# Kernel optimization log

Hardware: AMD Instinct MI355X
Metric: run time of the kernel (lower is better)

Reference implementation:

```python
import jax, jax.numpy as jnp
import numpy as np
from jax import lax

D_MODEL = 1024
STATE_DIM = 512
BATCH = 4
SEQ_LEN = 8192


def _cayley_eigenvalues(a_params, n):
    # a_full = [0, a_1..a_half, -a_half-1..., antisymmetric tail]
    half = n // 2
    a_full = jnp.zeros((n,), dtype=a_params.dtype)
    a_full = a_full.at[1:half + 1].set(a_params)
    a_full = a_full.at[half + 1:].set(-a_params[::-1][: n - half - 1])
    a_hat = jnp.fft.fft(a_full)            # complex64
    omega = jnp.imag(a_hat)                # (n,), float32
    ones = jnp.ones_like(omega)
    num = lax.complex(ones, -omega)
    den = lax.complex(ones, omega)
    return num / den                        # (n,), |lambda|=1


def setup_inputs() -> dict:
    key = jax.random.key(0)
    k1, k2, k3, k4 = jax.random.split(key, 4)
    u = jax.random.normal(k1, (BATCH, SEQ_LEN, D_MODEL), dtype=jnp.float32)
    a_params = jax.random.normal(k2, (STATE_DIM // 2,), dtype=jnp.float32) * 0.1
    # torch Linear weights: B.weight (state_dim, d_model), C.weight (d_model, state_dim)
    B_w = jax.random.normal(k3, (STATE_DIM, D_MODEL), dtype=jnp.float32) / np.sqrt(D_MODEL)
    C_w = jax.random.normal(k4, (D_MODEL, STATE_DIM), dtype=jnp.float32) / np.sqrt(STATE_DIM)
    D = jnp.ones((D_MODEL,), dtype=jnp.float32)
    return {"u": u, "a_params": a_params, "B_w": B_w, "C_w": C_w, "D": D}


def reference(u, a_params, B_w, C_w, D):
    batch, seq_len, d = u.shape
    n = B_w.shape[0]
    # 1) input projection: (b, t, n)
    Bu = jnp.einsum("btd,nd->btn", u, B_w)
    # 2) per-channel geometric kernel k_j[t] = lambda_j^t
    eig = _cayley_eigenvalues(a_params, n)                 # (n,) complex64
    t = jnp.arange(seq_len, dtype=jnp.float32)
    kernel = jnp.exp(t[:, None] * jnp.log(eig)[None, :])   # (T, n) complex64
    # 3) causal convolution via FFT with next-pow2(2T) padding
    fft_len = 1
    while fft_len < 2 * seq_len:
        fft_len *= 2
    pad = fft_len - seq_len
    kernel_padded = jnp.pad(kernel, ((0, pad), (0, 0)))
    K_hat = jnp.fft.fft(kernel_padded, axis=0)             # (F, n)
    Bu_padded = jnp.pad(Bu, ((0, 0), (0, pad), (0, 0))).astype(jnp.complex64)
    Bu_hat = jnp.fft.fft(Bu_padded, axis=1)                # (b, F, n)
    h = jnp.fft.ifft(K_hat[None] * Bu_hat, axis=1).real[:, :seq_len, :]
    # 4) output projection + skip
    y = jnp.einsum("btn,dn->btd", h, C_w) + D * u
    return y
```

## Files before the change

kernel.cpp:

```cpp
#include <hip/hip_runtime.h>
#include <cstdint>
#include <cstddef>

#define D_MODEL   1024
#define STATE_DIM 512
#define BATCH     4
#define SEQ_LEN   8192
#define M_TOTAL   (BATCH * SEQ_LEN)

typedef unsigned short ushort_t;
typedef __attribute__((ext_vector_type(8))) __bf16 bf16x8;
typedef __attribute__((ext_vector_type(4))) float  f32x4;


__device__ inline ushort_t f2bf(float f) {
  union { float f; uint32_t u; } v; v.f = f;
  uint32_t u = v.u;
  uint32_t r = (u + 0x7FFFu + ((u >> 16) & 1u)) >> 16;
  return (ushort_t)r;
}

__device__ inline float bf2f(ushort_t b) {
  union { uint32_t u; float f; } v; v.u = ((uint32_t)b) << 16;
  return v.f;
}

__device__ inline void llds16(const void* g, void* l) {
  __builtin_amdgcn_global_load_lds(
      (__attribute__((address_space(1))) void*)(void*)g,
      (__attribute__((address_space(3))) void*)l,
      16, 0, 0);
}


__global__ void convert_f32_bf16(const float* __restrict__ in,
                                 ushort_t* __restrict__ out, int n4) {
  int i = blockIdx.x * blockDim.x + threadIdx.x;
  if (i >= n4) return;
  const float4 v = ((const float4*)in)[i];
  ushort4 o;
  o.x = f2bf(v.x); o.y = f2bf(v.y); o.z = f2bf(v.z); o.w = f2bf(v.w);
  ((ushort4*)out)[i] = o;
}


#define NCHUNK 128
#define CLEN   64
#define SOFF   (BATCH * NCHUNK * STATE_DIM)

__global__ __launch_bounds__(64)
void eigen_kernel(const float* __restrict__ a_params, float* __restrict__ lam) {
  const int k = blockIdx.x;
  const int l = threadIdx.x;
  const float c = 6.283185307179586f / 512.0f;
  float om = 0.f;
#pragma unroll
  for (int s = 0; s < 8; ++s) {
    const int n = s * 64 + l;
    float v = 0.f;
    if (n >= 1 && n <= STATE_DIM / 2)      v = a_params[n - 1];
    else if (n > STATE_DIM / 2)            v = -a_params[STATE_DIM - n];
    const int p = (k * n) & 511;
    om -= v * sinf(c * (float)p);
  }
#pragma unroll
  for (int off = 32; off; off >>= 1) om += __shfl_down(om, off);
  if (l == 0) {
    const float d  = 1.f / (1.f + om * om);
    const float lr = (1.f - om * om) * d;
    const float li = -2.f * om * d;
    double th = atan2((double)li, (double)lr) * (double)CLEN;
    lam[k]        = lr;
    lam[512 + k]  = li;
    lam[1024 + k] = (float)cos(th);
    lam[1536 + k] = (float)sin(th);
  }
}


template <int KDIM, int NDIM, bool OUT_BF16, bool FUSE_SKIP>
__global__ __launch_bounds__(256, 4)
void gemm_bt(const ushort_t* __restrict__ A,
             const ushort_t* __restrict__ Bw,
             void* __restrict__ outv,
             const ushort_t* __restrict__ skip_b,
             const float* __restrict__ Dvec) {
  __shared__ __align__(16) ushort_t smA[2 * 128 * 32];
  __shared__ __align__(16) ushort_t smB[2 * 128 * 32];
  const int tid    = threadIdx.x;
  const int wave   = tid >> 6, lane = tid & 63;
  const int lane16 = lane & 15, quad = lane >> 4;
  const int wm = (wave & 1) * 64, wn = (wave >> 1) * 64;
  const int row0 = blockIdx.x * 128;
  const int col0 = blockIdx.y * 128;

  f32x4 acc[4][4];
#pragma unroll
  for (int i = 0; i < 4; ++i)
#pragma unroll
    for (int j = 0; j < 4; ++j) {
      f32x4 z = {0.f, 0.f, 0.f, 0.f};
      acc[i][j] = z;
    }

  const int s_r0 = tid >> 2;
  const int s_c0 = (tid & 3) ^ ((s_r0 >> 1) & 3);
  const int s_r1 = (256 + tid) >> 2;
  const int s_c1 = (tid & 3) ^ ((s_r1 >> 1) & 3);
  const int o0 = (wave * 64) * 16;
  const int o1 = (256 + wave * 64) * 16;

  const ushort_t* gA0 = A  + (size_t)(row0 + s_r0) * KDIM + s_c0 * 8;
  const ushort_t* gB0 = Bw + (size_t)(col0 + s_r0) * KDIM + s_c0 * 8;
  const ushort_t* gA1 = A  + (size_t)(row0 + s_r1) * KDIM + s_c1 * 8;
  const ushort_t* gB1 = Bw + (size_t)(col0 + s_r1) * KDIM + s_c1 * 8;

#define STAGE(k0, buf)                                                   \
  do {                                                                   \
    char* bA = (char*)(smA + (buf) * (128 * 32));                        \
    char* bB = (char*)(smB + (buf) * (128 * 32));                        \
    llds16(gA0 + (k0), bA + o0);                                         \
    llds16(gB0 + (k0), bB + o0);                                         \
    llds16(gA1 + (k0), bA + o1);                                         \
    llds16(gB1 + (k0), bB + o1);                                         \
  } while (0)

  STAGE(0, 0);
  __syncthreads();

  constexpr int NIT = KDIM / 32;
  int cur = 0;
#pragma unroll 2
  for (int it = 0; it < NIT; ++it) {
    if (it + 1 < NIT) STAGE((it + 1) * 32, cur ^ 1);

    const ushort_t* sA = smA + cur * (128 * 32);
    const ushort_t* sB = smB + cur * (128 * 32);
    bf16x8 af[4], bfr[4];
#pragma unroll
    for (int mi = 0; mi < 4; ++mi) {
      const int m = wm + mi * 16 + lane16;
      const int pc = quad ^ ((m >> 1) & 3);
      af[mi] = *(const bf16x8*)(sA + (m * 4 + pc) * 8);
    }
#pragma unroll
    for (int ni = 0; ni < 4; ++ni) {
      const int n = wn + ni * 16 + lane16;
      const int pc = quad ^ ((n >> 1) & 3);
      bfr[ni] = *(const bf16x8*)(sB + (n * 4 + pc) * 8);
    }
#pragma unroll
    for (int mi = 0; mi < 4; ++mi)
#pragma unroll
      for (int ni = 0; ni < 4; ++ni)
        acc[mi][ni] = __builtin_amdgcn_mfma_f32_16x16x32_bf16(
            af[mi], bfr[ni], acc[mi][ni], 0, 0, 0);

    __syncthreads();
    cur ^= 1;
  }
#undef STAGE

#pragma unroll
  for (int mi = 0; mi < 4; ++mi) {
#pragma unroll
    for (int ni = 0; ni < 4; ++ni) {
      const int row = row0 + wm + mi * 16 + quad * 4;
      const int col = col0 + wn + ni * 16 + lane16;
      float dv = 0.f;
      if (FUSE_SKIP) dv = Dvec[col];
#pragma unroll
      for (int r = 0; r < 4; ++r) {
        const size_t o = (size_t)(row + r) * NDIM + col;
        float val = acc[mi][ni][r];
        if (FUSE_SKIP) val = fmaf(dv, bf2f(skip_b[o]), val);
        if (OUT_BF16) ((ushort_t*)outv)[o] = f2bf(val);
        else          ((float*)outv)[o] = val;
      }
    }
  }
}


__global__ __launch_bounds__(128)
void scan_chunks(const ushort_t* __restrict__ Bu, const float* __restrict__ lam,
                 float* __restrict__ S) {
  const int j = threadIdx.x * 4;
  const int c = blockIdx.x & (NCHUNK - 1);
  const int b = blockIdx.x >> 7;
  float lr[4], li[4], hr[4] = {0,0,0,0}, hi[4] = {0,0,0,0};
#pragma unroll
  for (int q = 0; q < 4; ++q) { lr[q] = lam[j + q]; li[q] = lam[512 + j + q]; }
  const ushort_t* p = Bu + ((size_t)(b * SEQ_LEN + c * CLEN)) * STATE_DIM + j;
#pragma unroll 4
  for (int t = 0; t < CLEN; ++t) {
    const ushort4 x4 = *(const ushort4*)(p + (size_t)t * STATE_DIM);
    const float x[4] = {bf2f(x4.x), bf2f(x4.y), bf2f(x4.z), bf2f(x4.w)};
#pragma unroll
    for (int q = 0; q < 4; ++q) {
      const float nr = fmaf(lr[q], hr[q], fmaf(-li[q], hi[q], x[q]));
      const float ni = fmaf(lr[q], hi[q], li[q] * hr[q]);
      hr[q] = nr; hi[q] = ni;
    }
  }
  const size_t o = (size_t)(b * NCHUNK + c) * STATE_DIM + j;
#pragma unroll
  for (int q = 0; q < 4; ++q) { S[o + q] = hr[q]; S[SOFF + o + q] = hi[q]; }
}

__global__ __launch_bounds__(512)
void scan_carry(const float* __restrict__ lam, const float* __restrict__ S,
                float* __restrict__ Hin) {
  const int idx = blockIdx.x * blockDim.x + threadIdx.x;
  const int j = idx & 511, b = idx >> 9;
  const float pr = lam[1024 + j], pi = lam[1536 + j];
  float cr = 0.f, ci = 0.f;
  for (int c = 0; c < NCHUNK; ++c) {
    const size_t o = (size_t)(b * NCHUNK + c) * STATE_DIM + j;
    Hin[o] = cr; Hin[SOFF + o] = ci;
    const float sr = S[o], si = S[SOFF + o];
    const float nr = fmaf(pr, cr, fmaf(-pi, ci, sr));
    const float ni = fmaf(pr, ci, fmaf(pi, cr, si));
    cr = nr; ci = ni;
  }
}

__global__ __launch_bounds__(128)
void scan_final(const ushort_t* __restrict__ Bu, const float* __restrict__ lam,
                const float* __restrict__ Hin, ushort_t* __restrict__ h) {
  const int j = threadIdx.x * 4;
  const int c = blockIdx.x & (NCHUNK - 1);
  const int b = blockIdx.x >> 7;
  float lr[4], li[4], hr[4], hi[4];
#pragma unroll
  for (int q = 0; q < 4; ++q) { lr[q] = lam[j + q]; li[q] = lam[512 + j + q]; }
  const size_t so = (size_t)(b * NCHUNK + c) * STATE_DIM + j;
#pragma unroll
  for (int q = 0; q < 4; ++q) { hr[q] = Hin[so + q]; hi[q] = Hin[SOFF + so + q]; }
  const size_t base = ((size_t)(b * SEQ_LEN + c * CLEN)) * STATE_DIM + j;
#pragma unroll 4
  for (int t = 0; t < CLEN; ++t) {
    const ushort4 x4 = *(const ushort4*)(Bu + base + (size_t)t * STATE_DIM);
    const float x[4] = {bf2f(x4.x), bf2f(x4.y), bf2f(x4.z), bf2f(x4.w)};
    ushort4 o4;
#pragma unroll
    for (int q = 0; q < 4; ++q) {
      const float nr = fmaf(lr[q], hr[q], fmaf(-li[q], hi[q], x[q]));
      const float ni = fmaf(lr[q], hi[q], li[q] * hr[q]);
      hr[q] = nr; hi[q] = ni;
    }
    o4.x = f2bf(hr[0]); o4.y = f2bf(hr[1]); o4.z = f2bf(hr[2]); o4.w = f2bf(hr[3]);
    *(ushort4*)(h + base + (size_t)t * STATE_DIM) = o4;
  }
}


extern "C" void kernel_launch(void* const* d_in, const int* in_sizes, int n_in,
                              void* d_out, int out_size, void* d_ws, size_t ws_size,
                              hipStream_t stream) {
  const float* u  = (const float*)d_in[0];
  const float* ap = (const float*)d_in[1];
  const float* Bw = (const float*)d_in[2];
  const float* Cw = (const float*)d_in[3];
  const float* Dv = (const float*)d_in[4];
  float* y = (float*)d_out;

  char* ws = (char*)d_ws;
  ushort_t* ub  = (ushort_t*)(ws + 0);
  ushort_t* bwb = (ushort_t*)(ws + 67108864);
  ushort_t* cwb = (ushort_t*)(ws + 68157440);
  float*    lam = (float*)   (ws + 69206016);
  ushort_t* Bu  = (ushort_t*)(ws + 69214208);
  ushort_t* hb  = (ushort_t*)(ws + 102768640);
  float*    S   = (float*)   (ws + 136323072);
  float*    Hin = (float*)   (ws + 138420224);

  convert_f32_bf16<<<32768, 256, 0, stream>>>(u,  ub,  (M_TOTAL * D_MODEL) / 4);
  convert_f32_bf16<<<512,   256, 0, stream>>>(Bw, bwb, (STATE_DIM * D_MODEL) / 4);
  convert_f32_bf16<<<512,   256, 0, stream>>>(Cw, cwb, (D_MODEL * STATE_DIM) / 4);
  eigen_kernel<<<512, 64, 0, stream>>>(ap, lam);

  gemm_bt<D_MODEL, STATE_DIM, true, false>
      <<<dim3(M_TOTAL / 128, STATE_DIM / 128), 256, 0, stream>>>(
          ub, bwb, Bu, nullptr, nullptr);

  scan_chunks<<<BATCH * NCHUNK, 128, 0, stream>>>(Bu, lam, S);
  scan_carry<<<BATCH, 512, 0, stream>>>(lam, S, Hin);
  scan_final<<<BATCH * NCHUNK, 128, 0, stream>>>(Bu, lam, Hin, hb);

  gemm_bt<STATE_DIM, D_MODEL, false, true>
      <<<dim3(M_TOTAL / 128, D_MODEL / 128), 256, 0, stream>>>(
          hb, cwb, y, ub, Dv);
}
```

Baseline: 376.7 us.

## Fuse fp32-to-bf16 conversion of u into the input projection GEMM

```diff
diff --git a/kernel.cpp b/kernel.cpp
--- a/kernel.cpp
+++ b/kernel.cpp
@@ -74,6 +74,147 @@
     lam[512 + k]  = li;
     lam[1024 + k] = (float)cos(th);
     lam[1536 + k] = (float)sin(th);
+  }
+}
+
+
+__global__ __launch_bounds__(256, 3)
+void gemm1_fused(const float* __restrict__ u,
+                 const ushort_t* __restrict__ Bw,
+                 ushort_t* __restrict__ Bu,
+                 ushort_t* __restrict__ ub) {
+  constexpr int KDIM = D_MODEL, NDIM = STATE_DIM, NIT = KDIM / 32;
+  __shared__ __align__(16) ushort_t smA[2 * 128 * 32];
+  __shared__ __align__(16) ushort_t smB[2 * 128 * 32];
+  const int tid    = threadIdx.x;
+  const int wave   = tid >> 6, lane = tid & 63;
+  const int lane16 = lane & 15, quad = lane >> 4;
+  const int wm = (wave & 1) * 64, wn = (wave >> 1) * 64;
+  const int row0 = blockIdx.x * 128;
+  const int col0 = blockIdx.y * 128;
+  const bool dost = (blockIdx.y == (blockIdx.x & 3));
+
+  f32x4 acc[4][4];
+#pragma unroll
+  for (int i = 0; i < 4; ++i)
+#pragma unroll
+    for (int j = 0; j < 4; ++j) {
+      f32x4 z = {0.f, 0.f, 0.f, 0.f};
+      acc[i][j] = z;
+    }
+
+  const int ar = tid >> 1, h = tid & 1;
+  const int pA = (ar >> 1) & 3;
+  const int ab0 = ar * 64 + (((2 * h)     ^ pA) << 4);
+  const int ab1 = ar * 64 + (((2 * h + 1) ^ pA) << 4);
+  const float*   gAa = u  + (size_t)(row0 + ar) * KDIM + h * 16;
+  ushort_t*      ubp = ub + (size_t)(row0 + ar) * KDIM + h * 16;
+
+  const int s_r0 = tid >> 2;
+  const int s_c0 = (tid & 3) ^ ((s_r0 >> 1) & 3);
+  const int s_r1 = 64 + s_r0;
+  const int s_c1 = (tid & 3) ^ ((s_r1 >> 1) & 3);
+  const ushort_t* gB0 = Bw + (size_t)(col0 + s_r0) * KDIM + s_c0 * 8;
+  const ushort_t* gB1 = Bw + (size_t)(col0 + s_r1) * KDIM + s_c1 * 8;
+  const int o0 = wave * 1024, o1 = 4096 + wave * 1024;
+
+#define STAGEB(kt, buf)                                                  \
+  do {                                                                   \
+    char* bB = (char*)smB + (buf) * 8192;                                \
+    llds16(gB0 + (kt) * 32, bB + o0);                                    \
+    llds16(gB1 + (kt) * 32, bB + o1);                                    \
+  } while (0)
+
+  f32x4 rA[4], rB[4];
+#define A_LDG(R, kt)                                                     \
+  do {                                                                   \
+    const float* _p = gAa + (size_t)(kt) * 32;                           \
+    _Pragma("unroll") for (int i = 0; i < 4; ++i) R[i] = *(const f32x4*)(_p + i * 4); \
+  } while (0)
+
+#define A_PUT(R, buf, kt)                                                \
+  do {                                                                   \
+    bf16x8 c0, c1;                                                       \
+    _Pragma("unroll") for (int i = 0; i < 8; ++i) {                      \
+      c0[i] = (__bf16)R[i >> 2][i & 3];                                  \
+      c1[i] = (__bf16)R[2 + (i >> 2)][i & 3];                            \
+    }                                                                    \
+    char* bA = (char*)smA + (buf) * 8192;                                \
+    *(bf16x8*)(bA + ab0) = c0;                                           \
+    *(bf16x8*)(bA + ab1) = c1;                                           \
+    if (dost) {                                                          \
+      *(bf16x8*)(ubp + (size_t)(kt) * 32)     = c0;                      \
+      *(bf16x8*)(ubp + (size_t)(kt) * 32 + 8) = c1;                      \
+    }                                                                    \
+  } while (0)
+
+#define COMPUTE(CUR)                                                     \
+  do {                                                                   \
+    const ushort_t* sA = smA + (CUR) * 4096;                             \
+    const ushort_t* sB = smB + (CUR) * 4096;                             \
+    bf16x8 af[4], bfr[4];                                                \
+    _Pragma("unroll") for (int mi = 0; mi < 4; ++mi) {                   \
+      const int m = wm + mi * 16 + lane16;                               \
+      const int pc = quad ^ ((m >> 1) & 3);                              \
+      af[mi] = *(const bf16x8*)(sA + (m * 4 + pc) * 8);                  \
+    }                                                                    \
+    _Pragma("unroll") for (int ni = 0; ni < 4; ++ni) {                   \
+      const int n = wn + ni * 16 + lane16;                               \
+      const int pc = quad ^ ((n >> 1) & 3);                              \
+      bfr[ni] = *(const bf16x8*)(sB + (n * 4 + pc) * 8);                 \
+    }                                                                    \
+    _Pragma("unroll") for (int mi = 0; mi < 4; ++mi)                     \
+      _Pragma("unroll") for (int ni = 0; ni < 4; ++ni)                   \
+        acc[mi][ni] = __builtin_amdgcn_mfma_f32_16x16x32_bf16(           \
+            af[mi], bfr[ni], acc[mi][ni], 0, 0, 0);                      \
+  } while (0)
+
+#define GBAR(keep4)                                                      \
+  do {                                                                   \
+    if (keep4) asm volatile("s_waitcnt vmcnt(4) lgkmcnt(0)" ::: "memory"); \
+    else       asm volatile("s_waitcnt vmcnt(0) lgkmcnt(0)" ::: "memory"); \
+    __builtin_amdgcn_sched_barrier(0);                                   \
+    __builtin_amdgcn_s_barrier();                                        \
+    asm volatile("" ::: "memory");                                       \
+    __builtin_amdgcn_sched_barrier(0);                                   \
+  } while (0)
+
+  A_LDG(rA, 0);
+  STAGEB(0, 0);
+  A_LDG(rB, 1);
+  A_PUT(rA, 0, 0);
+  A_LDG(rA, 2);
+  __syncthreads();
+
+#pragma unroll 1
+  for (int it = 0; it < NIT; it += 2) {
+    if (it + 1 < NIT) { STAGEB(it + 1, 1); A_PUT(rB, 1, it + 1); }
+    if (it + 3 < NIT) A_LDG(rB, it + 3);
+    COMPUTE(0);
+    GBAR(it + 3 < NIT);
+    if (it + 2 < NIT) { STAGEB(it + 2, 0); A_PUT(rA, 0, it + 2); }
+    if (it + 4 < NIT) A_LDG(rA, it + 4);
+    COMPUTE(1);
+    GBAR(it + 4 < NIT);
+  }
+#undef GBAR
+#undef COMPUTE
+#undef A_PUT
+#undef A_LDG
+#undef STAGEB
+
+#pragma unroll
+  for (int mi = 0; mi < 4; ++mi) {
+#pragma unroll
+    for (int ni = 0; ni < 4; ++ni) {
+      const int row = row0 + wm + mi * 16 + quad * 4;
+      const int col = col0 + wn + ni * 16 + lane16;
+#pragma unroll
+      for (int r = 0; r < 4; ++r) {
+        const size_t o = (size_t)(row + r) * NDIM + col;
+        Bu[o] = f2bf(acc[mi][ni][r]);
+      }
+    }
   }
 }
 
@@ -275,14 +416,12 @@
   float*    S   = (float*)   (ws + 136323072);
   float*    Hin = (float*)   (ws + 138420224);
 
-  convert_f32_bf16<<<32768, 256, 0, stream>>>(u,  ub,  (M_TOTAL * D_MODEL) / 4);
-  convert_f32_bf16<<<512,   256, 0, stream>>>(Bw, bwb, (STATE_DIM * D_MODEL) / 4);
-  convert_f32_bf16<<<512,   256, 0, stream>>>(Cw, cwb, (D_MODEL * STATE_DIM) / 4);
+  convert_f32_bf16<<<512, 256, 0, stream>>>(Bw, bwb, (STATE_DIM * D_MODEL) / 4);
+  convert_f32_bf16<<<512, 256, 0, stream>>>(Cw, cwb, (D_MODEL * STATE_DIM) / 4);
   eigen_kernel<<<512, 64, 0, stream>>>(ap, lam);
 
-  gemm_bt<D_MODEL, STATE_DIM, true, false>
-      <<<dim3(M_TOTAL / 128, STATE_DIM / 128), 256, 0, stream>>>(
-          ub, bwb, Bu, nullptr, nullptr);
+  gemm1_fused<<<dim3(M_TOTAL / 128, STATE_DIM / 128), 256, 0, stream>>>(
+      u, bwb, Bu, ub);
 
   scan_chunks<<<BATCH * NCHUNK, 128, 0, stream>>>(Bu, lam, S);
   scan_carry<<<BATCH, 512, 0, stream>>>(lam, S, Hin);
```

New measurement: 443.0 us. 1.18x slower.
